# Performance work log

Hardware: AMD Instinct MI355X
Metric: run time of the kernel (lower is better)

The kernel has to match this reference:

```python
import jax, jax.numpy as jnp
import numpy as np
from jax.scipy.special import logsumexp

B, S, H, L = 64, 512, 1024, 9  # batch, seq_len, hidden_size, num_labels


def setup_inputs() -> dict:
    key = jax.random.key(0)
    ks = jax.random.split(key, 6)
    inputs = jax.random.normal(ks[0], (B, S, H), jnp.float32)
    labels = jax.random.randint(ks[1], (B, S), 0, L).astype(jnp.int64)
    mask = jnp.ones((B, S), jnp.int32)
    # fc parameters (nn.Linear(hidden_size, num_labels))
    W = jax.random.normal(ks[2], (L, H), jnp.float32) / np.sqrt(H)
    b = jnp.zeros((L,), jnp.float32)
    # CRF parameters (include_start_end_trans=True)
    trans_m = jax.random.normal(ks[3], (L, L), jnp.float32) * 0.1
    start_scores = jax.random.normal(ks[4], (L,), jnp.float32) * 0.1
    end_scores = jax.random.normal(ks[5], (L,), jnp.float32) * 0.1
    return dict(inputs=inputs, labels=labels, mask=mask, W=W, b=b,
                trans_m=trans_m, start_scores=start_scores, end_scores=end_scores)


def _crf_nll_mean(inputs, W, b, trans_m, start_scores, end_scores, labels, mask):
    # logits = fc(inputs): [B, S, L]
    logits = jnp.einsum('bsh,lh->bsl', inputs, W) + b
    feats = jnp.swapaxes(logits, 0, 1)           # [S, B, L] (fastNLP transposes)
    tags = jnp.swapaxes(labels, 0, 1)            # [S, B]
    m = jnp.swapaxes(mask, 0, 1).astype(feats.dtype)  # [S, B]
    seq_len, batch, n_tags = feats.shape

    # ---- log-partition via forward algorithm (lax.scan over time) ----
    alpha0 = feats[0] + start_scores[None, :]    # [B, L]

    def step(alpha, x):
        emit, mt = x                              # emit: [B, L], mt: [B]
        # tmp[b, i, j] = alpha[b, i] + trans_m[i, j] + emit[b, j]
        tmp = alpha[:, :, None] + trans_m[None, :, :] + emit[:, None, :]
        new = logsumexp(tmp, axis=1)              # [B, L]
        alpha = jnp.where(mt[:, None] > 0, new, alpha)
        return alpha, None

    alpha, _ = jax.lax.scan(step, alpha0, (feats[1:], m[1:]))
    norm = logsumexp(alpha + end_scores[None, :], axis=1)   # [B]

    # ---- gold path score ----
    emit = jnp.take_along_axis(feats, tags[:, :, None], axis=2)[:, :, 0] * m  # [S, B]
    trans = trans_m[tags[:-1], tags[1:]] * m[1:]                               # [S-1, B]
    score = emit.sum(0) + trans.sum(0)                                         # [B]
    last_idx = m.sum(0).astype(jnp.int32) - 1                                  # [B]
    last_tags = tags[last_idx, jnp.arange(batch)]
    score = score + start_scores[tags[0]] + end_scores[last_tags]

    # loss = crf(logits, labels, mask).mean()
    return jnp.mean(norm - score)


def reference(inputs, labels, mask, W, b, trans_m, start_scores, end_scores):
    return _crf_nll_mean(inputs, W, b, trans_m, start_scores, end_scores, labels, mask)
```

## Files before the change

kernel.cpp:

```cpp
#include <hip/hip_runtime.h>
#include <hip/hip_bf16.h>


#define BATCH 64
#define SEQ   512
#define HID   1024
#define NLAB  9
#define CHUNK 32
#define NCHUNK (SEQ / CHUNK)
#define NREC (BATCH * NCHUNK * NLAB)
#define NROWS (BATCH * SEQ)
#define NTILES (NROWS / 16)

__device__ __forceinline__ float exp2_fast(float x) { return __builtin_amdgcn_exp2f(x); }
__device__ __forceinline__ float log2_fast(float x) { return __builtin_amdgcn_logf(x); }

#define LOG2E 1.4426950408889634f
#define LN2   0.6931471805599453f

typedef __attribute__((ext_vector_type(8))) short short8;
typedef __attribute__((ext_vector_type(4))) float float4v;

__global__ __launch_bounds__(256) void wcvt_kernel(
    const float* __restrict__ W, __hip_bfloat16* __restrict__ wbf)
{
    int idx = blockIdx.x * 256 + threadIdx.x;
    int n = idx >> 10, k = idx & 1023;
    float v = (n < NLAB) ? W[n * HID + k] * LOG2E : 0.0f;
    wbf[idx] = __float2bfloat16(v);
}

__global__ __launch_bounds__(256) void logits_kernel(
    const float* __restrict__ inp, const __hip_bfloat16* __restrict__ wbf,
    const float* __restrict__ bias, float* __restrict__ feats)
{
    const int lane = threadIdx.x & 63;
    const int wv   = threadIdx.x >> 6;
    const int wid  = blockIdx.x * 4 + wv;
    const int n    = lane & 15;
    const int q8   = lane >> 4;
    const long r0  = (long)wid * 32;

    const float* a0p = inp + (r0 + n) * HID + q8 * 8;
    const float* a1p = a0p + 16 * HID;
    const short* bp  = (const short*)wbf + n * HID + q8 * 8;

    float4v acc0 = {0.f, 0.f, 0.f, 0.f};
    float4v acc1 = {0.f, 0.f, 0.f, 0.f};

    for (int kk = 0; kk < 32; ++kk) {
        const int ko = kk * 32;
        float x0[8], x1[8];
        *(float4*)(x0)     = *(const float4*)(a0p + ko);
        *(float4*)(x0 + 4) = *(const float4*)(a0p + ko + 4);
        *(float4*)(x1)     = *(const float4*)(a1p + ko);
        *(float4*)(x1 + 4) = *(const float4*)(a1p + ko + 4);
        short8 bfrag = *(const short8*)(bp + ko);

        short8 af0, af1;
        #pragma unroll
        for (int j = 0; j < 8; ++j) {
            union { __hip_bfloat16 h; short s; } u0, u1;
            u0.h = __float2bfloat16(x0[j]);
            u1.h = __float2bfloat16(x1[j]);
            af0[j] = u0.s;
            af1[j] = u1.s;
        }
        acc0 = __builtin_amdgcn_mfma_f32_16x16x32_bf16(af0, bfrag, acc0, 0, 0, 0);
        acc1 = __builtin_amdgcn_mfma_f32_16x16x32_bf16(af1, bfrag, acc1, 0, 0, 0);
    }

    if (n < NLAB) {
        const float bK = bias[n] * LOG2E;
        #pragma unroll
        for (int r = 0; r < 4; ++r) {
            const long row = r0 + q8 * 4 + r;
            feats[row * NLAB + n]        = acc0[r] + bK;
            feats[(row + 16) * NLAB + n] = acc1[r] + bK;
        }
    }
}

__global__ __launch_bounds__(64) void chunk_kernel(
    const float* __restrict__ feats, const float* __restrict__ trans,
    const int* __restrict__ mask, float* __restrict__ P,
    float* __restrict__ out)
{
    const int lane = threadIdx.x;
    if (blockIdx.x == 0 && lane == 63) out[0] = 0.0f;
    const int g = lane / 9;
    const int j = lane - g * 9;
    int rid = blockIdx.x * 7 + g;
    bool act = (g < 7) && (rid < NREC);
    if (!act) rid = 0;

    const int i  = rid % NLAB;
    const int bc = rid / NLAB;
    const int c  = bc & (NCHUNK - 1);
    const int b  = bc >> 4;

    float tr[NLAB];
    #pragma unroll
    for (int k = 0; k < NLAB; ++k) tr[k] = trans[k * NLAB + j] * LOG2E;
    const float tri = trans[i * NLAB + j] * LOG2E;

    const float* fb = feats + (long)b * SEQ * NLAB;
    const int* mb = mask + b * SEQ;
    const int ts = (c == 0) ? 1 : c * CHUNK;
    const int te = (c + 1) * CHUNK;
    const int sbase = g * 9;

    float a;
    {
        int m0 = mb[ts];
        float e0 = fb[ts * NLAB + j];
        float aid = (i == j) ? 0.0f : -1e30f;
        a = (m0 > 0) ? (tri + e0) : aid;
    }

    float e_nxt = fb[(ts + 1) * NLAB + j];
    int   m_nxt = mb[ts + 1];
    for (int t = ts + 1; t < te; ++t) {
        float e = e_nxt;
        int  mt = m_nxt;
        if (t + 1 < te) {
            e_nxt = fb[(t + 1) * NLAB + j];
            m_nxt = mb[t + 1];
        }
        float v[NLAB];
        #pragma unroll
        for (int k = 0; k < NLAB; ++k) v[k] = __shfl(a, sbase + k, 64) + tr[k];
        float m01 = fmaxf(v[0], v[1]), m23 = fmaxf(v[2], v[3]);
        float m45 = fmaxf(v[4], v[5]), m67 = fmaxf(v[6], v[7]);
        float mx = fmaxf(fmaxf(fmaxf(m01, m23), fmaxf(m45, m67)), v[8]);
        float s = 0.0f;
        #pragma unroll
        for (int k = 0; k < NLAB; ++k) s += exp2_fast(v[k] - mx);
        float an = mx + log2_fast(s) + e;
        a = (mt > 0) ? an : a;
    }
    if (act) P[(long)rid * NLAB + j] = a;
}

__global__ __launch_bounds__(64) void final_kernel(
    const float* __restrict__ feats, const float* __restrict__ trans,
    const float* __restrict__ startv, const float* __restrict__ endv,
    const int* __restrict__ labels, const int* __restrict__ mask,
    const float* __restrict__ P, float* __restrict__ out)
{
    const int b = blockIdx.x, lane = threadIdx.x;
    const float* fb = feats + (long)b * SEQ * NLAB;
    const int* lb = labels + b * SEQ;
    const int* mb = mask + b * SEQ;

    float gsum = 0.0f; int msum = 0;
    for (int t = lane; t < SEQ; t += 64) {
        int tag = lb[t];
        int mt = mb[t];
        if (mt > 0) {
            gsum += fb[t * NLAB + tag];
            msum++;
            if (t > 0) gsum += trans[lb[t - 1] * NLAB + tag] * LOG2E;
        }
    }
    #pragma unroll
    for (int off = 32; off > 0; off >>= 1) {
        gsum += __shfl_xor(gsum, off, 64);
        msum += __shfl_xor(msum, off, 64);
    }

    const int j = lane % 9;
    float al = fb[j] + startv[j] * LOG2E;
    const float* Pb = P + (long)b * NCHUNK * 81;
    float pc[NLAB];
    #pragma unroll
    for (int i = 0; i < NLAB; ++i) pc[i] = Pb[i * NLAB + j];
    #pragma unroll
    for (int c = 0; c < NCHUNK; ++c) {
        float pn[NLAB];
        if (c < NCHUNK - 1) {
            #pragma unroll
            for (int i = 0; i < NLAB; ++i) pn[i] = Pb[(c + 1) * 81 + i * NLAB + j];
        } else {
            #pragma unroll
            for (int i = 0; i < NLAB; ++i) pn[i] = 0.0f;
        }
        float v[NLAB];
        #pragma unroll
        for (int i = 0; i < NLAB; ++i) v[i] = __shfl(al, i, 64) + pc[i];
        float m01 = fmaxf(v[0], v[1]), m23 = fmaxf(v[2], v[3]);
        float m45 = fmaxf(v[4], v[5]), m67 = fmaxf(v[6], v[7]);
        float mx = fmaxf(fmaxf(fmaxf(m01, m23), fmaxf(m45, m67)), v[8]);
        float s = 0.0f;
        #pragma unroll
        for (int i = 0; i < NLAB; ++i) s += exp2_fast(v[i] - mx);
        al = mx + log2_fast(s);
        #pragma unroll
        for (int i = 0; i < NLAB; ++i) pc[i] = pn[i];
    }
    al += endv[j] * LOG2E;

    float v[NLAB];
    #pragma unroll
    for (int i = 0; i < NLAB; ++i) v[i] = __shfl(al, i, 64);
    float m01 = fmaxf(v[0], v[1]), m23 = fmaxf(v[2], v[3]);
    float m45 = fmaxf(v[4], v[5]), m67 = fmaxf(v[6], v[7]);
    float mx = fmaxf(fmaxf(fmaxf(m01, m23), fmaxf(m45, m67)), v[8]);
    float s = 0.0f;
    #pragma unroll
    for (int i = 0; i < NLAB; ++i) s += exp2_fast(v[i] - mx);
    float norm = mx + log2_fast(s);

    if (lane == 0) {
        int li = (msum > 0) ? (msum - 1) : 0;
        float score = gsum + startv[lb[0]] * LOG2E + endv[lb[li]] * LOG2E;
        atomicAdd(out, (norm - score) * (LN2 / (float)BATCH));
    }
}

extern "C" void kernel_launch(void* const* d_in, const int* in_sizes, int n_in,
                              void* d_out, int out_size, void* d_ws, size_t ws_size,
                              hipStream_t stream)
{
    const float* inp    = (const float*)d_in[0];
    const int*   labels = (const int*)d_in[1];
    const int*   mask   = (const int*)d_in[2];
    const float* W      = (const float*)d_in[3];
    const float* bias   = (const float*)d_in[4];
    const float* trans  = (const float*)d_in[5];
    const float* startv = (const float*)d_in[6];
    const float* endv   = (const float*)d_in[7];

    float* feats = (float*)d_ws;
    float* P     = feats + (long)NROWS * NLAB;
    __hip_bfloat16* wbf = (__hip_bfloat16*)(P + (long)BATCH * NCHUNK * 81);
    float* out   = (float*)d_out;

    hipLaunchKernelGGL(wcvt_kernel, dim3(64), dim3(256), 0, stream, W, wbf);
    hipLaunchKernelGGL(logits_kernel, dim3(NTILES / 8), dim3(256), 0, stream,
                       inp, wbf, bias, feats);
    hipLaunchKernelGGL(chunk_kernel, dim3((NREC + 6) / 7), dim3(64), 0, stream,
                       feats, trans, mask, P, out);
    hipLaunchKernelGGL(final_kernel, dim3(BATCH), dim3(64), 0, stream,
                       feats, trans, startv, endv, labels, mask, P, out);
}
```

Baseline: 237.6 us.

## Run chunk transfer products in linear space with one row per thread

The chunk kernel now gives each thread a whole row of the chunk transfer matrix. It updates that row in linear space as a 9x9 matrix-vector product with precomputed exp(trans), rescales by a power of two via frexp/ldexp, and takes the log only at the end. This removes the per-step cross-lane shuffles and the nine exp plus one log per element of each step. Feats are padded to a 12-float stride so each step's emissions load as three float4 reads, and the logits kernel uses one MFMA tile per wave with twice as many blocks. Underflow for extreme emission ranges is a risk, since nr entries are exp2 of emissions times a normalized row.

```diff
diff --git a/kernel.cpp b/kernel.cpp
--- a/kernel.cpp
+++ b/kernel.cpp
@@ -6,6 +6,7 @@
 #define SEQ   512
 #define HID   1024
 #define NLAB  9
+#define FST   12
 #define CHUNK 32
 #define NCHUNK (SEQ / CHUNK)
 #define NREC (BATCH * NCHUNK * NLAB)
@@ -22,12 +23,18 @@
 typedef __attribute__((ext_vector_type(4))) float float4v;
 
 __global__ __launch_bounds__(256) void wcvt_kernel(
-    const float* __restrict__ W, __hip_bfloat16* __restrict__ wbf)
+    const float* __restrict__ W, const float* __restrict__ trans,
+    __hip_bfloat16* __restrict__ wbf, float* __restrict__ T2,
+    float* __restrict__ out)
 {
     int idx = blockIdx.x * 256 + threadIdx.x;
     int n = idx >> 10, k = idx & 1023;
     float v = (n < NLAB) ? W[n * HID + k] * LOG2E : 0.0f;
     wbf[idx] = __float2bfloat16(v);
+    if (blockIdx.x == 0) {
+        if (threadIdx.x < 81) T2[threadIdx.x] = exp2_fast(trans[threadIdx.x] * LOG2E);
+        if (threadIdx.x == 81) out[0] = 0.0f;
+    }
 }
 
 __global__ __launch_bounds__(256) void logits_kernel(
@@ -39,107 +46,108 @@
     const int wid  = blockIdx.x * 4 + wv;
     const int n    = lane & 15;
     const int q8   = lane >> 4;
-    const long r0  = (long)wid * 32;
-
-    const float* a0p = inp + (r0 + n) * HID + q8 * 8;
-    const float* a1p = a0p + 16 * HID;
-    const short* bp  = (const short*)wbf + n * HID + q8 * 8;
-
-    float4v acc0 = {0.f, 0.f, 0.f, 0.f};
-    float4v acc1 = {0.f, 0.f, 0.f, 0.f};
+    const long r0  = (long)wid * 16;
+
+    const float* ap = inp + (r0 + n) * HID + q8 * 8;
+    const short* bp = (const short*)wbf + n * HID + q8 * 8;
+
+    float4v acc = {0.f, 0.f, 0.f, 0.f};
 
     for (int kk = 0; kk < 32; ++kk) {
         const int ko = kk * 32;
-        float x0[8], x1[8];
-        *(float4*)(x0)     = *(const float4*)(a0p + ko);
-        *(float4*)(x0 + 4) = *(const float4*)(a0p + ko + 4);
-        *(float4*)(x1)     = *(const float4*)(a1p + ko);
-        *(float4*)(x1 + 4) = *(const float4*)(a1p + ko + 4);
+        float x[8];
+        *(float4*)(x)     = *(const float4*)(ap + ko);
+        *(float4*)(x + 4) = *(const float4*)(ap + ko + 4);
         short8 bfrag = *(const short8*)(bp + ko);
-
-        short8 af0, af1;
+        short8 af;
         #pragma unroll
         for (int j = 0; j < 8; ++j) {
-            union { __hip_bfloat16 h; short s; } u0, u1;
-            u0.h = __float2bfloat16(x0[j]);
-            u1.h = __float2bfloat16(x1[j]);
-            af0[j] = u0.s;
-            af1[j] = u1.s;
-        }
-        acc0 = __builtin_amdgcn_mfma_f32_16x16x32_bf16(af0, bfrag, acc0, 0, 0, 0);
-        acc1 = __builtin_amdgcn_mfma_f32_16x16x32_bf16(af1, bfrag, acc1, 0, 0, 0);
-    }
-
-    if (n < NLAB) {
-        const float bK = bias[n] * LOG2E;
+            union { __hip_bfloat16 h; short s; } u;
+            u.h = __float2bfloat16(x[j]);
+            af[j] = u.s;
+        }
+        acc = __builtin_amdgcn_mfma_f32_16x16x32_bf16(af, bfrag, acc, 0, 0, 0);
+    }
+
+    if (n < FST) {
+        const float bK = (n < NLAB) ? bias[n] * LOG2E : 0.0f;
         #pragma unroll
         for (int r = 0; r < 4; ++r) {
             const long row = r0 + q8 * 4 + r;
-            feats[row * NLAB + n]        = acc0[r] + bK;
-            feats[(row + 16) * NLAB + n] = acc1[r] + bK;
+            feats[row * FST + n] = (n < NLAB) ? (acc[r] + bK) : 0.0f;
         }
     }
 }
 
 __global__ __launch_bounds__(64) void chunk_kernel(
-    const float* __restrict__ feats, const float* __restrict__ trans,
-    const int* __restrict__ mask, float* __restrict__ P,
-    float* __restrict__ out)
-{
-    const int lane = threadIdx.x;
-    if (blockIdx.x == 0 && lane == 63) out[0] = 0.0f;
-    const int g = lane / 9;
-    const int j = lane - g * 9;
-    int rid = blockIdx.x * 7 + g;
-    bool act = (g < 7) && (rid < NREC);
-    if (!act) rid = 0;
-
+    const float* __restrict__ feats, const float* __restrict__ T2,
+    const int* __restrict__ mask, float* __restrict__ P)
+{
+    const int rid = blockIdx.x * 64 + threadIdx.x;
     const int i  = rid % NLAB;
     const int bc = rid / NLAB;
     const int c  = bc & (NCHUNK - 1);
     const int b  = bc >> 4;
 
-    float tr[NLAB];
-    #pragma unroll
-    for (int k = 0; k < NLAB; ++k) tr[k] = trans[k * NLAB + j] * LOG2E;
-    const float tri = trans[i * NLAB + j] * LOG2E;
-
-    const float* fb = feats + (long)b * SEQ * NLAB;
+    float T[NLAB][NLAB];
+    #pragma unroll
+    for (int k = 0; k < NLAB; ++k)
+        #pragma unroll
+        for (int j = 0; j < NLAB; ++j) T[k][j] = T2[k * NLAB + j];
+
+    const float* fb = feats + (long)b * SEQ * FST;
     const int* mb = mask + b * SEQ;
-    const int ts = (c == 0) ? 1 : c * CHUNK;
-    const int te = (c + 1) * CHUNK;
-    const int sbase = g * 9;
-
-    float a;
+    const int t0 = c * CHUNK;
+    const int ts = (c == 0) ? 1 : t0;
+    const int te = t0 + CHUNK;
+
+    float row[NLAB];
+    #pragma unroll
+    for (int k = 0; k < NLAB; ++k) row[k] = (k == i) ? 1.0f : 0.0f;
+    float shift = 0.0f;
+
+    float e[12]; int m_cur;
     {
-        int m0 = mb[ts];
-        float e0 = fb[ts * NLAB + j];
-        float aid = (i == j) ? 0.0f : -1e30f;
-        a = (m0 > 0) ? (tri + e0) : aid;
-    }
-
-    float e_nxt = fb[(ts + 1) * NLAB + j];
-    int   m_nxt = mb[ts + 1];
-    for (int t = ts + 1; t < te; ++t) {
-        float e = e_nxt;
-        int  mt = m_nxt;
+        const float4* p = (const float4*)(fb + (long)ts * FST);
+        *(float4*)(e) = p[0]; *(float4*)(e + 4) = p[1]; *(float4*)(e + 8) = p[2];
+        m_cur = mb[ts];
+    }
+
+    for (int t = ts; t < te; ++t) {
+        float en[12]; int m_nxt = 0;
         if (t + 1 < te) {
-            e_nxt = fb[(t + 1) * NLAB + j];
+            const float4* p = (const float4*)(fb + (long)(t + 1) * FST);
+            *(float4*)(en) = p[0]; *(float4*)(en + 4) = p[1]; *(float4*)(en + 8) = p[2];
             m_nxt = mb[t + 1];
         }
-        float v[NLAB];
-        #pragma unroll
-        for (int k = 0; k < NLAB; ++k) v[k] = __shfl(a, sbase + k, 64) + tr[k];
-        float m01 = fmaxf(v[0], v[1]), m23 = fmaxf(v[2], v[3]);
-        float m45 = fmaxf(v[4], v[5]), m67 = fmaxf(v[6], v[7]);
-        float mx = fmaxf(fmaxf(fmaxf(m01, m23), fmaxf(m45, m67)), v[8]);
-        float s = 0.0f;
-        #pragma unroll
-        for (int k = 0; k < NLAB; ++k) s += exp2_fast(v[k] - mx);
-        float an = mx + log2_fast(s) + e;
-        a = (mt > 0) ? an : a;
-    }
-    if (act) P[(long)rid * NLAB + j] = a;
+        float nr[NLAB];
+        #pragma unroll
+        for (int j = 0; j < NLAB; ++j) {
+            float a = row[0] * T[0][j];
+            #pragma unroll
+            for (int k = 1; k < NLAB; ++k) a = fmaf(row[k], T[k][j], a);
+            nr[j] = a * exp2_fast(e[j]);
+        }
+        float mx = nr[0];
+        #pragma unroll
+        for (int j = 1; j < NLAB; ++j) mx = fmaxf(mx, nr[j]);
+        int ex = __builtin_amdgcn_frexp_expf(mx);
+        const bool upd = (m_cur > 0);
+        #pragma unroll
+        for (int j = 0; j < NLAB; ++j) {
+            float sj = __builtin_amdgcn_ldexpf(nr[j], -ex);
+            row[j] = upd ? sj : row[j];
+        }
+        shift = upd ? (shift + (float)ex) : shift;
+
+        #pragma unroll
+        for (int q = 0; q < 12; ++q) e[q] = en[q];
+        m_cur = m_nxt;
+    }
+
+    float* Pp = P + (long)rid * NLAB;
+    #pragma unroll
+    for (int j = 0; j < NLAB; ++j) Pp[j] = log2_fast(row[j]) + shift;
 }
 
 __global__ __launch_bounds__(64) void final_kernel(
@@ -149,7 +157,7 @@
     const float* __restrict__ P, float* __restrict__ out)
 {
     const int b = blockIdx.x, lane = threadIdx.x;
-    const float* fb = feats + (long)b * SEQ * NLAB;
+    const float* fb = feats + (long)b * SEQ * FST;
     const int* lb = labels + b * SEQ;
     const int* mb = mask + b * SEQ;
 
@@ -158,7 +166,7 @@
         int tag = lb[t];
         int mt = mb[t];
         if (mt > 0) {
-            gsum += fb[t * NLAB + tag];
+            gsum += fb[t * FST + tag];
             msum++;
             if (t > 0) gsum += trans[lb[t - 1] * NLAB + tag] * LOG2E;
         }
@@ -232,15 +240,17 @@
     const float* endv   = (const float*)d_in[7];
 
     float* feats = (float*)d_ws;
-    float* P     = feats + (long)NROWS * NLAB;
-    __hip_bfloat16* wbf = (__hip_bfloat16*)(P + (long)BATCH * NCHUNK * 81);
+    float* P     = feats + (long)NROWS * FST;
+    float* T2    = P + (long)BATCH * NCHUNK * 81;
+    __hip_bfloat16* wbf = (__hip_bfloat16*)(T2 + 128);
     float* out   = (float*)d_out;
 
-    hipLaunchKernelGGL(wcvt_kernel, dim3(64), dim3(256), 0, stream, W, wbf);
-    hipLaunchKernelGGL(logits_kernel, dim3(NTILES / 8), dim3(256), 0, stream,
+    hipLaunchKernelGGL(wcvt_kernel, dim3(64), dim3(256), 0, stream,
+                       W, trans, wbf, T2, out);
+    hipLaunchKernelGGL(logits_kernel, dim3(NTILES / 4), dim3(256), 0, stream,
                        inp, wbf, bias, feats);
-    hipLaunchKernelGGL(chunk_kernel, dim3((NREC + 6) / 7), dim3(64), 0, stream,
-                       feats, trans, mask, P, out);
+    hipLaunchKernelGGL(chunk_kernel, dim3(NREC / 64), dim3(64), 0, stream,
+                       feats, T2, mask, P);
     hipLaunchKernelGGL(final_kernel, dim3(BATCH), dim3(64), 0, stream,
                        feats, trans, startv, endv, labels, mask, P, out);
 }
```

Result: slower. 244.8 us (+3.0%).
